# Kernel tuning notes

Hardware: AMD Instinct MI355X
Metric: run time of the kernel (lower is better)

## Reference

```python
import jax, jax.numpy as jnp
import numpy as np

N, D, C = 100000, 384, 8


def setup_inputs() -> dict:
    key = jax.random.key(0)
    k1, k2, k3, k4 = jax.random.split(key, 4)
    Y = jax.random.normal(k1, (N, D), dtype=jnp.float32)
    O = jax.random.bernoulli(k2, 0.9, (N, D))  # observation mask
    # learned VB parameters (as held in the nn.Parameters of VBPCA)
    mbar = 0.1 * jax.random.normal(k3, (D,), dtype=jnp.float32)
    wbar = 0.1 * jax.random.normal(k4, (D, C), dtype=jnp.float32)
    Sigmaw = jnp.broadcast_to(jnp.eye(C, dtype=jnp.float32), (D, C, C))
    vy = jnp.float32(1.0)
    return {"Y": Y, "O": O, "mbar": mbar, "wbar": wbar, "Sigmaw": Sigmaw, "vy": vy}


def reference(Y, O, mbar, wbar, Sigmaw, vy):
    O_ = O.astype(Y.dtype)            # [N, D]
    Y = jnp.nan_to_num(Y)
    # per-channel rank-c outer product plus Sigmaw: baddbmm(Sigmaw, wbar[:,:,None], wbar[:,None,:])
    OwwSw = Sigmaw + wbar[:, :, None] * wbar[:, None, :]            # [D, C, C]
    # accumulate over observed channels: [N, D] @ [D, C*C] -> [N, C, C]
    A = (O_ @ OwwSw.reshape(D, C * C)).reshape(-1, C, C)
    Ic = jnp.eye(C, dtype=Y.dtype)
    Sigma_xn = vy * jnp.linalg.inv(vy * Ic[None] + A)               # [N, C, C]
    # xbarn = einsum('nlk,ni,ik,ni->nl', Sigma_xn/vy, O_, wbar, Y - mbar)
    t = O_ * (Y - mbar)                                             # [N, D]
    proj = t @ wbar                                                 # [N, C]
    xbarn = jnp.einsum('nlk,nk->nl', Sigma_xn / vy, proj)           # [N, C]
    return xbarn, Sigma_xn
```

## Files before the change

### kernel.cpp

```cpp
#include <hip/hip_runtime.h>

#define NN 100000
#define DD 384
#define CC 8
#define ROWS 64

typedef unsigned int uint;
typedef _Float16 half8 __attribute__((ext_vector_type(8)));
typedef float floatx4 __attribute__((ext_vector_type(4)));

__device__ __forceinline__ constexpr int TIDX(int i, int j) { return i * (i + 1) / 2 + j; }

__device__ __forceinline__ uint pkh2(float a, float b) {
  return __builtin_bit_cast(uint, __builtin_amdgcn_cvt_pkrtz(a, b));
}

__global__ __launch_bounds__(64) void vbpca_prep(
    const float* __restrict__ wbar, const float* __restrict__ Sigmaw,
    uint4* __restrict__ bfrag) {
  const int l = threadIdx.x;
  const int kt = blockIdx.x;
  const int kgrp = l >> 4;
#pragma unroll
  for (int ct = 0; ct < 3; ++ct) {
    const int col = ct * 16 + (l & 15);
    int ii = 0;
#pragma unroll
    for (int t = 0; t < 7; ++t) {
      if ((ii + 1) * (ii + 2) / 2 <= col && ii < 7) ++ii;
    }
    const int jj = col - ii * (ii + 1) / 2;
    float v[8];
#pragma unroll
    for (int j = 0; j < 8; ++j) {
      const int d = kt * 32 + kgrp * 8 + j;
      float val;
      if (col < 36) {
        val = Sigmaw[(size_t)d * 64 + ii * 8 + jj] + wbar[d * 8 + ii] * wbar[d * 8 + jj];
      } else if (col < 44) {
        val = wbar[d * 8 + (col - 36)];
      } else {
        val = 0.f;
      }
      v[j] = val;
    }
    uint4 u;
    u.x = pkh2(v[0], v[1]); u.y = pkh2(v[2], v[3]);
    u.z = pkh2(v[4], v[5]); u.w = pkh2(v[6], v[7]);
    bfrag[(kt * 3 + ct) * 64 + l] = u;
  }
}

__global__ __launch_bounds__(256, 5) void vbpca_main(
    const float* __restrict__ Y, const int* __restrict__ O,
    const uint4* __restrict__ bfrag, const float* __restrict__ mbar,
    const float* __restrict__ vyp, float* __restrict__ out) {
  __shared__ float smemf[6656];
  float* mbar_l = smemf;
  uint* tile_l = (uint*)(smemf + 384);
  float* scat_l = smemf + 384;

  const int tid = threadIdx.x;
  const int l = tid & 63;
  const int w = tid >> 6;

  for (int i = tid; i < DD; i += 256) mbar_l[i] = mbar[i];

  const int lrow0 = tid >> 3;
  const int c4 = tid & 7;
  int rg0 = blockIdx.x * ROWS + lrow0;
  if (rg0 >= NN) rg0 = NN - 1;
  int rg1 = blockIdx.x * ROWS + lrow0 + 32;
  if (rg1 >= NN) rg1 = NN - 1;

  float4 y0, y1;
  int4 o0, o1;
#define ISSUE(KT)                                                          \
  {                                                                        \
    const size_t off0 = (size_t)rg0 * DD + (KT) * 32 + c4 * 4;             \
    const size_t off1 = (size_t)rg1 * DD + (KT) * 32 + c4 * 4;             \
    y0 = *reinterpret_cast<const float4*>(Y + off0);                       \
    o0 = *reinterpret_cast<const int4*>(O + off0);                         \
    y1 = *reinterpret_cast<const float4*>(Y + off1);                       \
    o1 = *reinterpret_cast<const int4*>(O + off1);                         \
  }

  ISSUE(0);

  floatx4 acc[2][3];
#pragma unroll
  for (int i = 0; i < 2; ++i)
#pragma unroll
    for (int j = 0; j < 3; ++j) acc[i][j] = (floatx4){0.f, 0.f, 0.f, 0.f};

  __syncthreads();

  for (int kt = 0; kt < 12; ++kt) {
    {
      const float4 mb = *reinterpret_cast<const float4*>(mbar_l + kt * 32 + c4 * 4);
      {
        const float f0 = (float)o0.x, f1 = (float)o0.y, f2 = (float)o0.z, f3 = (float)o0.w;
        uint* b0 = tile_l + (2 * lrow0) * 16 + c4 * 2;
        b0[0] = pkh2(f0, f1);
        b0[1] = pkh2(f2, f3);
        uint* b1 = tile_l + (2 * lrow0 + 1) * 16 + c4 * 2;
        b1[0] = pkh2(f0 * (y0.x - mb.x), f1 * (y0.y - mb.y));
        b1[1] = pkh2(f2 * (y0.z - mb.z), f3 * (y0.w - mb.w));
      }
      {
        const float f0 = (float)o1.x, f1 = (float)o1.y, f2 = (float)o1.z, f3 = (float)o1.w;
        uint* b0 = tile_l + (2 * (lrow0 + 32)) * 16 + c4 * 2;
        b0[0] = pkh2(f0, f1);
        b0[1] = pkh2(f2, f3);
        uint* b1 = tile_l + (2 * (lrow0 + 32) + 1) * 16 + c4 * 2;
        b1[0] = pkh2(f0 * (y1.x - mb.x), f1 * (y1.y - mb.y));
        b1[1] = pkh2(f2 * (y1.z - mb.z), f3 * (y1.w - mb.w));
      }
    }
    if (kt < 11) ISSUE(kt + 1);
    __syncthreads();

    {
      const int rt0 = 2 * w, rt1 = 2 * w + 1;
      const half8 a0 = *reinterpret_cast<const half8*>(
          tile_l + (rt0 * 16 + (l & 15)) * 16 + (l >> 4) * 4);
      const half8 a1 = *reinterpret_cast<const half8*>(
          tile_l + (rt1 * 16 + (l & 15)) * 16 + (l >> 4) * 4);
      const uint4 B0 = bfrag[(kt * 3 + 0) * 64 + l];
      const uint4 B1 = bfrag[(kt * 3 + 1) * 64 + l];
      const uint4 B2 = bfrag[(kt * 3 + 2) * 64 + l];
      const half8 b0 = __builtin_bit_cast(half8, B0);
      const half8 b1 = __builtin_bit_cast(half8, B1);
      const half8 b2 = __builtin_bit_cast(half8, B2);
      acc[0][0] = __builtin_amdgcn_mfma_f32_16x16x32_f16(a0, b0, acc[0][0], 0, 0, 0);
      acc[0][1] = __builtin_amdgcn_mfma_f32_16x16x32_f16(a0, b1, acc[0][1], 0, 0, 0);
      acc[0][2] = __builtin_amdgcn_mfma_f32_16x16x32_f16(a0, b2, acc[0][2], 0, 0, 0);
      acc[1][0] = __builtin_amdgcn_mfma_f32_16x16x32_f16(a1, b0, acc[1][0], 0, 0, 0);
      acc[1][1] = __builtin_amdgcn_mfma_f32_16x16x32_f16(a1, b1, acc[1][1], 0, 0, 0);
      acc[1][2] = __builtin_amdgcn_mfma_f32_16x16x32_f16(a1, b2, acc[1][2], 0, 0, 0);
    }
    __syncthreads();
  }

#pragma unroll
  for (int rtl = 0; rtl < 2; ++rtl) {
    const int rt = 2 * w + rtl;
#pragma unroll
    for (int ct = 0; ct < 3; ++ct) {
#pragma unroll
      for (int reg = 0; reg < 4; ++reg) {
        scat_l[(rt * 16 + (l >> 4) * 4 + reg) * 49 + ct * 16 + (l & 15)] =
            acc[rtl][ct][reg];
      }
    }
  }
  __syncthreads();
  if (tid >= 64) return;

  const int row = tid;
  const int grow = blockIdx.x * ROWS + row;

  float a[36], pr[CC];
#pragma unroll
  for (int k = 0; k < 36; ++k) a[k] = scat_l[(2 * row) * 49 + k];
#pragma unroll
  for (int j = 0; j < CC; ++j) pr[j] = scat_l[(2 * row + 1) * 49 + 36 + j];

  const float vy = *vyp;

  float L[36];
#pragma unroll
  for (int j = 0; j < CC; ++j) {
    float s = a[TIDX(j, j)] + vy;
#pragma unroll
    for (int k = 0; k < CC; ++k) {
      if (k < j) s -= L[TIDX(j, k)] * L[TIDX(j, k)];
    }
    const float dj = sqrtf(s);
    L[TIDX(j, j)] = dj;
    const float invdj = 1.0f / dj;
#pragma unroll
    for (int i = j + 1; i < CC; ++i) {
      float tt = a[TIDX(i, j)];
#pragma unroll
      for (int k = 0; k < CC; ++k) {
        if (k < j) tt -= L[TIDX(i, k)] * L[TIDX(j, k)];
      }
      L[TIDX(i, j)] = tt * invdj;
    }
  }

  float invd[CC];
#pragma unroll
  for (int i = 0; i < CC; ++i) invd[i] = 1.0f / L[TIDX(i, i)];
  float Li[36];
#pragma unroll
  for (int j = 0; j < CC; ++j) {
    Li[TIDX(j, j)] = invd[j];
#pragma unroll
    for (int i = j + 1; i < CC; ++i) {
      float s = 0.f;
#pragma unroll
      for (int k = 0; k < CC; ++k) {
        if (k >= j && k < i) s += L[TIDX(i, k)] * Li[TIDX(k, j)];
      }
      Li[TIDX(i, j)] = -s * invd[i];
    }
  }

  float sig[36];
#pragma unroll
  for (int i = 0; i < CC; ++i) {
#pragma unroll
    for (int j = 0; j <= i; ++j) {
      float s = 0.f;
#pragma unroll
      for (int k = 0; k < CC; ++k) {
        if (k >= i) s += Li[TIDX(k, i)] * Li[TIDX(k, j)];
      }
      sig[TIDX(i, j)] = vy * s;
    }
  }

  float uvec[CC];
#pragma unroll
  for (int i = 0; i < CC; ++i) {
    float s = 0.f;
#pragma unroll
    for (int j = 0; j < CC; ++j) {
      if (j <= i) s += Li[TIDX(i, j)] * pr[j];
    }
    uvec[i] = s;
  }
  float xb[CC];
#pragma unroll
  for (int ll = 0; ll < CC; ++ll) {
    float s = 0.f;
#pragma unroll
    for (int i = 0; i < CC; ++i) {
      if (i >= ll) s += Li[TIDX(i, ll)] * uvec[i];
    }
    xb[ll] = s;
  }

  if (grow >= NN) return;

  float4* __restrict__ xo = reinterpret_cast<float4*>(out + (size_t)grow * CC);
  xo[0] = make_float4(xb[0], xb[1], xb[2], xb[3]);
  xo[1] = make_float4(xb[4], xb[5], xb[6], xb[7]);

  float4* __restrict__ so4 =
      reinterpret_cast<float4*>(out + (size_t)NN * CC + (size_t)grow * 64);
#pragma unroll
  for (int i = 0; i < CC; ++i) {
    float rowv[CC];
#pragma unroll
    for (int j = 0; j < CC; ++j) {
      rowv[j] = (j <= i) ? sig[TIDX(i, j)] : sig[TIDX(j, i)];
    }
    so4[i * 2 + 0] = make_float4(rowv[0], rowv[1], rowv[2], rowv[3]);
    so4[i * 2 + 1] = make_float4(rowv[4], rowv[5], rowv[6], rowv[7]);
  }
}

extern "C" void kernel_launch(void* const* d_in, const int* in_sizes, int n_in,
                              void* d_out, int out_size, void* d_ws, size_t ws_size,
                              hipStream_t stream) {
  const float* Y = (const float*)d_in[0];
  const int* O = (const int*)d_in[1];
  const float* mbar = (const float*)d_in[2];
  const float* wbar = (const float*)d_in[3];
  const float* Sigmaw = (const float*)d_in[4];
  const float* vyp = (const float*)d_in[5];
  float* out = (float*)d_out;
  uint4* bfrag = (uint4*)d_ws;

  vbpca_prep<<<12, 64, 0, stream>>>(wbar, Sigmaw, bfrag);
  vbpca_main<<<(NN + ROWS - 1) / ROWS, 256, 0, stream>>>(Y, O, bfrag, mbar, vyp, out);
}
```

Baseline: 92.52 us.

## Double-buffer the LDS tile, pad rows, and stage outputs through LDS for coalesced stores

The K loop is unrolled by two with two LDS tile buffers and two sets of prefetch registers, so global loads for stage k+2 are in flight while stage k is packed and multiplied, and one barrier per stage is removed. Tile rows are padded from 16 to 20 words to reduce LDS bank conflicts on the MFMA fragment reads. The per-row Sigma and xbar results are written to LDS and then stored by all 256 threads in a contiguous, coalesced pattern, replacing scattered per-thread float4 stores from only 64 threads. This costs more registers and LDS, which may reduce occupancy, plus extra barriers in the epilogue.

Result: slower. 100.8 us (+9.0%).

```diff
diff --git a/kernel.cpp b/kernel.cpp
--- a/kernel.cpp
+++ b/kernel.cpp
@@ -59,6 +59,8 @@
   float* mbar_l = smemf;
   uint* tile_l = (uint*)(smemf + 384);
   float* scat_l = smemf + 384;
+  float* sigst = smemf + 384;
+  float* xbst = smemf + 384 + 4160;
 
   const int tid = threadIdx.x;
   const int l = tid & 63;
@@ -73,19 +75,41 @@
   int rg1 = blockIdx.x * ROWS + lrow0 + 32;
   if (rg1 >= NN) rg1 = NN - 1;
 
-  float4 y0, y1;
-  int4 o0, o1;
-#define ISSUE(KT)                                                          \
+  float4 yA0, yA1, yB0, yB1;
+  int4 oA0, oA1, oB0, oB1;
+#define ISSUE(S0y, S0o, S1y, S1o, KT)                                      \
   {                                                                        \
     const size_t off0 = (size_t)rg0 * DD + (KT) * 32 + c4 * 4;             \
     const size_t off1 = (size_t)rg1 * DD + (KT) * 32 + c4 * 4;             \
-    y0 = *reinterpret_cast<const float4*>(Y + off0);                       \
-    o0 = *reinterpret_cast<const int4*>(O + off0);                         \
-    y1 = *reinterpret_cast<const float4*>(Y + off1);                       \
-    o1 = *reinterpret_cast<const int4*>(O + off1);                         \
-  }
-
-  ISSUE(0);
+    S0y = *reinterpret_cast<const float4*>(Y + off0);                      \
+    S0o = *reinterpret_cast<const int4*>(O + off0);                        \
+    S1y = *reinterpret_cast<const float4*>(Y + off1);                      \
+    S1o = *reinterpret_cast<const int4*>(O + off1);                        \
+  }
+
+#define PACK(S0y, S0o, S1y, S1o, KT, BUF)                                   \
+  {                                                                         \
+    const float4 mb = *reinterpret_cast<const float4*>(mbar_l + (KT)*32 + c4 * 4); \
+    uint* tb = tile_l + (BUF)*2560;                                         \
+    {                                                                       \
+      const float f0 = (float)S0o.x, f1 = (float)S0o.y;                     \
+      const float f2 = (float)S0o.z, f3 = (float)S0o.w;                     \
+      uint* b0 = tb + (2 * lrow0) * 20 + c4 * 2;                            \
+      b0[0] = pkh2(f0, f1); b0[1] = pkh2(f2, f3);                           \
+      uint* b1 = tb + (2 * lrow0 + 1) * 20 + c4 * 2;                        \
+      b1[0] = pkh2(f0 * (S0y.x - mb.x), f1 * (S0y.y - mb.y));               \
+      b1[1] = pkh2(f2 * (S0y.z - mb.z), f3 * (S0y.w - mb.w));               \
+    }                                                                       \
+    {                                                                       \
+      const float f0 = (float)S1o.x, f1 = (float)S1o.y;                     \
+      const float f2 = (float)S1o.z, f3 = (float)S1o.w;                     \
+      uint* b0 = tb + (2 * (lrow0 + 32)) * 20 + c4 * 2;                     \
+      b0[0] = pkh2(f0, f1); b0[1] = pkh2(f2, f3);                           \
+      uint* b1 = tb + (2 * (lrow0 + 32) + 1) * 20 + c4 * 2;                 \
+      b1[0] = pkh2(f0 * (S1y.x - mb.x), f1 * (S1y.y - mb.y));               \
+      b1[1] = pkh2(f2 * (S1y.z - mb.z), f3 * (S1y.w - mb.w));               \
+    }                                                                       \
+  }
 
   floatx4 acc[2][3];
 #pragma unroll
@@ -93,54 +117,40 @@
 #pragma unroll
     for (int j = 0; j < 3; ++j) acc[i][j] = (floatx4){0.f, 0.f, 0.f, 0.f};
 
-  __syncthreads();
-
-  for (int kt = 0; kt < 12; ++kt) {
-    {
-      const float4 mb = *reinterpret_cast<const float4*>(mbar_l + kt * 32 + c4 * 4);
-      {
-        const float f0 = (float)o0.x, f1 = (float)o0.y, f2 = (float)o0.z, f3 = (float)o0.w;
-        uint* b0 = tile_l + (2 * lrow0) * 16 + c4 * 2;
-        b0[0] = pkh2(f0, f1);
-        b0[1] = pkh2(f2, f3);
-        uint* b1 = tile_l + (2 * lrow0 + 1) * 16 + c4 * 2;
-        b1[0] = pkh2(f0 * (y0.x - mb.x), f1 * (y0.y - mb.y));
-        b1[1] = pkh2(f2 * (y0.z - mb.z), f3 * (y0.w - mb.w));
-      }
-      {
-        const float f0 = (float)o1.x, f1 = (float)o1.y, f2 = (float)o1.z, f3 = (float)o1.w;
-        uint* b0 = tile_l + (2 * (lrow0 + 32)) * 16 + c4 * 2;
-        b0[0] = pkh2(f0, f1);
-        b0[1] = pkh2(f2, f3);
-        uint* b1 = tile_l + (2 * (lrow0 + 32) + 1) * 16 + c4 * 2;
-        b1[0] = pkh2(f0 * (y1.x - mb.x), f1 * (y1.y - mb.y));
-        b1[1] = pkh2(f2 * (y1.z - mb.z), f3 * (y1.w - mb.w));
-      }
-    }
-    if (kt < 11) ISSUE(kt + 1);
+#define MFMA_PHASE(KT, BUF)                                                 \
+  {                                                                         \
+    const uint* tb = tile_l + (BUF)*2560;                                   \
+    const half8 a0 = *reinterpret_cast<const half8*>(                       \
+        tb + ((2 * w) * 16 + (l & 15)) * 20 + (l >> 4) * 4);                \
+    const half8 a1 = *reinterpret_cast<const half8*>(                       \
+        tb + ((2 * w + 1) * 16 + (l & 15)) * 20 + (l >> 4) * 4);            \
+    const half8 b0 = __builtin_bit_cast(half8, bfrag[((KT)*3 + 0) * 64 + l]); \
+    const half8 b1 = __builtin_bit_cast(half8, bfrag[((KT)*3 + 1) * 64 + l]); \
+    const half8 b2 = __builtin_bit_cast(half8, bfrag[((KT)*3 + 2) * 64 + l]); \
+    acc[0][0] = __builtin_amdgcn_mfma_f32_16x16x32_f16(a0, b0, acc[0][0], 0, 0, 0); \
+    acc[0][1] = __builtin_amdgcn_mfma_f32_16x16x32_f16(a0, b1, acc[0][1], 0, 0, 0); \
+    acc[0][2] = __builtin_amdgcn_mfma_f32_16x16x32_f16(a0, b2, acc[0][2], 0, 0, 0); \
+    acc[1][0] = __builtin_amdgcn_mfma_f32_16x16x32_f16(a1, b0, acc[1][0], 0, 0, 0); \
+    acc[1][1] = __builtin_amdgcn_mfma_f32_16x16x32_f16(a1, b1, acc[1][1], 0, 0, 0); \
+    acc[1][2] = __builtin_amdgcn_mfma_f32_16x16x32_f16(a1, b2, acc[1][2], 0, 0, 0); \
+  }
+
+  ISSUE(yA0, oA0, yA1, oA1, 0);
+  ISSUE(yB0, oB0, yB1, oB1, 1);
+  __syncthreads();
+
+#pragma unroll 1
+  for (int kt = 0; kt < 12; kt += 2) {
+    PACK(yA0, oA0, yA1, oA1, kt, 0);
+    if (kt + 2 < 12) ISSUE(yA0, oA0, yA1, oA1, kt + 2);
     __syncthreads();
-
-    {
-      const int rt0 = 2 * w, rt1 = 2 * w + 1;
-      const half8 a0 = *reinterpret_cast<const half8*>(
-          tile_l + (rt0 * 16 + (l & 15)) * 16 + (l >> 4) * 4);
-      const half8 a1 = *reinterpret_cast<const half8*>(
-          tile_l + (rt1 * 16 + (l & 15)) * 16 + (l >> 4) * 4);
-      const uint4 B0 = bfrag[(kt * 3 + 0) * 64 + l];
-      const uint4 B1 = bfrag[(kt * 3 + 1) * 64 + l];
-      const uint4 B2 = bfrag[(kt * 3 + 2) * 64 + l];
-      const half8 b0 = __builtin_bit_cast(half8, B0);
-      const half8 b1 = __builtin_bit_cast(half8, B1);
-      const half8 b2 = __builtin_bit_cast(half8, B2);
-      acc[0][0] = __builtin_amdgcn_mfma_f32_16x16x32_f16(a0, b0, acc[0][0], 0, 0, 0);
-      acc[0][1] = __builtin_amdgcn_mfma_f32_16x16x32_f16(a0, b1, acc[0][1], 0, 0, 0);
-      acc[0][2] = __builtin_amdgcn_mfma_f32_16x16x32_f16(a0, b2, acc[0][2], 0, 0, 0);
-      acc[1][0] = __builtin_amdgcn_mfma_f32_16x16x32_f16(a1, b0, acc[1][0], 0, 0, 0);
-      acc[1][1] = __builtin_amdgcn_mfma_f32_16x16x32_f16(a1, b1, acc[1][1], 0, 0, 0);
-      acc[1][2] = __builtin_amdgcn_mfma_f32_16x16x32_f16(a1, b2, acc[1][2], 0, 0, 0);
-    }
+    MFMA_PHASE(kt, 0);
+    PACK(yB0, oB0, yB1, oB1, kt + 1, 1);
+    if (kt + 3 < 12) ISSUE(yB0, oB0, yB1, oB1, kt + 3);
     __syncthreads();
-  }
+    MFMA_PHASE(kt + 1, 1);
+  }
+  __syncthreads();
 
 #pragma unroll
   for (int rtl = 0; rtl < 2; ++rtl) {
@@ -155,111 +165,111 @@
     }
   }
   __syncthreads();
-  if (tid >= 64) return;
-
-  const int row = tid;
-  const int grow = blockIdx.x * ROWS + row;
 
   float a[36], pr[CC];
-#pragma unroll
-  for (int k = 0; k < 36; ++k) a[k] = scat_l[(2 * row) * 49 + k];
-#pragma unroll
-  for (int j = 0; j < CC; ++j) pr[j] = scat_l[(2 * row + 1) * 49 + 36 + j];
-
-  const float vy = *vyp;
-
-  float L[36];
-#pragma unroll
-  for (int j = 0; j < CC; ++j) {
-    float s = a[TIDX(j, j)] + vy;
-#pragma unroll
-    for (int k = 0; k < CC; ++k) {
-      if (k < j) s -= L[TIDX(j, k)] * L[TIDX(j, k)];
-    }
-    const float dj = sqrtf(s);
-    L[TIDX(j, j)] = dj;
-    const float invdj = 1.0f / dj;
-#pragma unroll
-    for (int i = j + 1; i < CC; ++i) {
-      float tt = a[TIDX(i, j)];
+  if (tid < 64) {
+#pragma unroll
+    for (int k = 0; k < 36; ++k) a[k] = scat_l[(2 * tid) * 49 + k];
+#pragma unroll
+    for (int j = 0; j < CC; ++j) pr[j] = scat_l[(2 * tid + 1) * 49 + 36 + j];
+  }
+  __syncthreads();
+
+  if (tid < 64) {
+    const int row = tid;
+    const float vy = *vyp;
+
+    float L[36];
+#pragma unroll
+    for (int j = 0; j < CC; ++j) {
+      float s = a[TIDX(j, j)] + vy;
 #pragma unroll
       for (int k = 0; k < CC; ++k) {
-        if (k < j) tt -= L[TIDX(i, k)] * L[TIDX(j, k)];
-      }
-      L[TIDX(i, j)] = tt * invdj;
-    }
-  }
-
-  float invd[CC];
-#pragma unroll
-  for (int i = 0; i < CC; ++i) invd[i] = 1.0f / L[TIDX(i, i)];
-  float Li[36];
-#pragma unroll
-  for (int j = 0; j < CC; ++j) {
-    Li[TIDX(j, j)] = invd[j];
-#pragma unroll
-    for (int i = j + 1; i < CC; ++i) {
+        if (k < j) s -= L[TIDX(j, k)] * L[TIDX(j, k)];
+      }
+      const float dj = sqrtf(s);
+      L[TIDX(j, j)] = dj;
+      const float invdj = 1.0f / dj;
+#pragma unroll
+      for (int i = j + 1; i < CC; ++i) {
+        float tt = a[TIDX(i, j)];
+#pragma unroll
+        for (int k = 0; k < CC; ++k) {
+          if (k < j) tt -= L[TIDX(i, k)] * L[TIDX(j, k)];
+        }
+        L[TIDX(i, j)] = tt * invdj;
+      }
+    }
+
+    float invd[CC];
+#pragma unroll
+    for (int i = 0; i < CC; ++i) invd[i] = 1.0f / L[TIDX(i, i)];
+    float Li[36];
+#pragma unroll
+    for (int j = 0; j < CC; ++j) {
+      Li[TIDX(j, j)] = invd[j];
+#pragma unroll
+      for (int i = j + 1; i < CC; ++i) {
+        float s = 0.f;
+#pragma unroll
+        for (int k = 0; k < CC; ++k) {
+          if (k >= j && k < i) s += L[TIDX(i, k)] * Li[TIDX(k, j)];
+        }
+        Li[TIDX(i, j)] = -s * invd[i];
+      }
+    }
+
+    float sig[36];
+#pragma unroll
+    for (int i = 0; i < CC; ++i) {
+#pragma unroll
+      for (int j = 0; j <= i; ++j) {
+        float s = 0.f;
+#pragma unroll
+        for (int k = 0; k < CC; ++k) {
+          if (k >= i) s += Li[TIDX(k, i)] * Li[TIDX(k, j)];
+        }
+        sig[TIDX(i, j)] = vy * s;
+      }
+    }
+
+    float uvec[CC];
+#pragma unroll
+    for (int i = 0; i < CC; ++i) {
       float s = 0.f;
 #pragma unroll
-      for (int k = 0; k < CC; ++k) {
-        if (k >= j && k < i) s += L[TIDX(i, k)] * Li[TIDX(k, j)];
-      }
-      Li[TIDX(i, j)] = -s * invd[i];
-    }
-  }
-
-  float sig[36];
-#pragma unroll
-  for (int i = 0; i < CC; ++i) {
-#pragma unroll
-    for (int j = 0; j <= i; ++j) {
+      for (int j = 0; j < CC; ++j) {
+        if (j <= i) s += Li[TIDX(i, j)] * pr[j];
+      }
+      uvec[i] = s;
+    }
+#pragma unroll
+    for (int ll = 0; ll < CC; ++ll) {
       float s = 0.f;
 #pragma unroll
-      for (int k = 0; k < CC; ++k) {
-        if (k >= i) s += Li[TIDX(k, i)] * Li[TIDX(k, j)];
-      }
-      sig[TIDX(i, j)] = vy * s;
-    }
-  }
-
-  float uvec[CC];
-#pragma unroll
-  for (int i = 0; i < CC; ++i) {
-    float s = 0.f;
-#pragma unroll
-    for (int j = 0; j < CC; ++j) {
-      if (j <= i) s += Li[TIDX(i, j)] * pr[j];
-    }
-    uvec[i] = s;
-  }
-  float xb[CC];
-#pragma unroll
-  for (int ll = 0; ll < CC; ++ll) {
-    float s = 0.f;
+      for (int i = 0; i < CC; ++i) {
+        if (i >= ll) s += Li[TIDX(i, ll)] * uvec[i];
+      }
+      xbst[row * 9 + ll] = s;
+    }
 #pragma unroll
     for (int i = 0; i < CC; ++i) {
-      if (i >= ll) s += Li[TIDX(i, ll)] * uvec[i];
-    }
-    xb[ll] = s;
-  }
-
-  if (grow >= NN) return;
-
-  float4* __restrict__ xo = reinterpret_cast<float4*>(out + (size_t)grow * CC);
-  xo[0] = make_float4(xb[0], xb[1], xb[2], xb[3]);
-  xo[1] = make_float4(xb[4], xb[5], xb[6], xb[7]);
-
-  float4* __restrict__ so4 =
-      reinterpret_cast<float4*>(out + (size_t)NN * CC + (size_t)grow * 64);
-#pragma unroll
-  for (int i = 0; i < CC; ++i) {
-    float rowv[CC];
-#pragma unroll
-    for (int j = 0; j < CC; ++j) {
-      rowv[j] = (j <= i) ? sig[TIDX(i, j)] : sig[TIDX(j, i)];
-    }
-    so4[i * 2 + 0] = make_float4(rowv[0], rowv[1], rowv[2], rowv[3]);
-    so4[i * 2 + 1] = make_float4(rowv[4], rowv[5], rowv[6], rowv[7]);
+#pragma unroll
+      for (int j = 0; j < CC; ++j) {
+        sigst[row * 65 + i * 8 + j] = (j <= i) ? sig[TIDX(i, j)] : sig[TIDX(j, i)];
+      }
+    }
+  }
+  __syncthreads();
+
+  const int valid = (NN - blockIdx.x * ROWS < ROWS) ? (NN - blockIdx.x * ROWS) : ROWS;
+  float* __restrict__ sig_out = out + (size_t)NN * CC + (size_t)blockIdx.x * ROWS * 64;
+  for (int f = tid; f < valid * 64; f += 256) {
+    sig_out[f] = sigst[(f >> 6) * 65 + (f & 63)];
+  }
+  float* __restrict__ xb_out = out + (size_t)blockIdx.x * ROWS * CC;
+  for (int f = tid; f < valid * 8; f += 256) {
+    xb_out[f] = xbst[(f >> 3) * 9 + (f & 7)];
   }
 }
 
```
